# Kernel tuning notes

Measured on AMD Instinct MI355X. Metric: run time of the kernel, lower is better.

The kernel has to match this reference:

```python
import jax, jax.numpy as jnp
import numpy as np
from jax import lax

T, H = 4096, 2048          # tokens, hidden_size
E, K = 64, 8               # n_routed_experts, top_k
I = 512                    # moe_intermediate_size
IS = 512                   # shared intermediate = moe_intermediate_size * n_shared_experts
ROUTED_SCALING = 2.5


def setup_inputs() -> dict:
    key = jax.random.key(0)
    ks = jax.random.split(key, 6)
    return {
        "hidden_states": jax.random.normal(ks[0], (T, H), jnp.float32),
        "gate_w": jax.random.normal(ks[1], (H, E), jnp.float32) * 0.05,
        "w13": jax.random.normal(ks[2], (E, H, 2 * I), jnp.float32) * 0.02,
        "w2": jax.random.normal(ks[3], (E, I, H), jnp.float32) * 0.02,
        "shared_w13": jax.random.normal(ks[4], (H, 2 * IS), jnp.float32) * 0.02,
        "shared_w2": jax.random.normal(ks[5], (IS, H), jnp.float32) * 0.02,
    }


def reference(hidden_states, gate_w, w13, w2, shared_w13, shared_w2):
    # --- router: sigmoid scoring, grouped top-k with 1 group == plain top-k ---
    logits = hidden_states @ gate_w                        # [T, E]
    scores = jax.nn.sigmoid(logits.astype(jnp.float32))
    topk_w, topk_ids = lax.top_k(scores, K)                # [T, K]
    topk_w = topk_w / jnp.sum(topk_w, axis=-1, keepdims=True)  # renormalize

    # --- dispatch: sort token-expert pairs by expert id, grouped GEMM ---
    flat_ids = topk_ids.reshape(-1)                        # [T*K]
    order = jnp.argsort(flat_ids)                          # pairs grouped by expert
    token_idx = order // K                                 # source token of each sorted pair
    x_sorted = hidden_states[token_idx]                    # [T*K, H]
    group_sizes = jnp.bincount(flat_ids, length=E).astype(jnp.int32)

    gu = lax.ragged_dot(x_sorted, w13, group_sizes)        # [T*K, 2I]
    h = jax.nn.silu(gu[:, :I]) * gu[:, I:]                 # SiluAndMul
    out_sorted = lax.ragged_dot(h, w2, group_sizes)        # [T*K, H]

    # --- combine: unsort, weight, sum over top-k ---
    inv = jnp.argsort(order)
    out_pairs = out_sorted[inv].reshape(T, K, H)
    routed = jnp.sum(out_pairs * topk_w[..., None].astype(out_pairs.dtype), axis=1)

    # --- shared expert MLP ---
    sg = hidden_states @ shared_w13                        # [T, 2*IS]
    shared = (jax.nn.silu(sg[:, :IS]) * sg[:, IS:]) @ shared_w2

    return routed * ROUTED_SCALING + shared
```

## Files before the change

kernel.cpp:

```cpp
#include <hip/hip_runtime.h>
#include <hip/hip_bf16.h>

#define T_TOK 4096
#define HD    2048
#define NE    64
#define TOPK  8
#define IMID  512
#define N13   1024
#define NPAIR (T_TOK*TOPK)
#define NROWS (NPAIR + T_TOK)
#define MAXT1 352
#define RSCALE 2.5f

typedef __attribute__((ext_vector_type(8)))  __bf16 bf16x8;
typedef __attribute__((ext_vector_type(4)))  __bf16 bf16x4;
typedef __attribute__((ext_vector_type(4)))  float  f32x4;


__global__ void init_small(int* __restrict__ counts, int* __restrict__ curs) {
  int tid = threadIdx.x;
  if (tid < NE + 1) { counts[tid] = 0; curs[tid] = 0; }
}
__global__ __launch_bounds__(256) void zero_out_kernel(float4* __restrict__ out4) {
  out4[blockIdx.x * 256 + threadIdx.x] = float4{0.f, 0.f, 0.f, 0.f};
}

__global__ __launch_bounds__(256) void logits_kernel(const float* __restrict__ hs,
                                                     const float* __restrict__ gw,
                                                     float* __restrict__ logits,
                                                     __bf16* __restrict__ hidden_bf) {
  __shared__ float hsm[64][16];
  __shared__ float gwm[64][64];
  int tid = threadIdx.x;
  int tb = blockIdx.x * 16;
  int tok = tid >> 4, e4 = (tid & 15) * 4;
  float acc[4] = {0.f, 0.f, 0.f, 0.f};
  for (int c = 0; c < 32; ++c) {
    int kb = c * 64;
    {
      int t16 = tid & 15, kq = tid >> 4;
      float4 f = *(const float4*)&hs[(size_t)(tb + t16) * HD + kb + kq * 4];
      hsm[kq * 4 + 0][t16] = f.x; hsm[kq * 4 + 1][t16] = f.y;
      hsm[kq * 4 + 2][t16] = f.z; hsm[kq * 4 + 3][t16] = f.w;
      bf16x4 hv = { (__bf16)f.x, (__bf16)f.y, (__bf16)f.z, (__bf16)f.w };
      *(bf16x4*)&hidden_bf[(size_t)(tb + t16) * HD + kb + kq * 4] = hv;
#pragma unroll
      for (int it = 0; it < 4; ++it) {
        int q = tid + it * 256;
        int gr = q >> 4, gc = (q & 15) * 4;
        *(float4*)&gwm[gr][gc] = *(const float4*)&gw[(size_t)(kb + gr) * NE + gc];
      }
    }
    __syncthreads();
#pragma unroll 8
    for (int k = 0; k < 64; ++k) {
      float h = hsm[k][tok];
      float4 g = *(const float4*)&gwm[k][e4];
      acc[0] += h * g.x; acc[1] += h * g.y; acc[2] += h * g.z; acc[3] += h * g.w;
    }
    __syncthreads();
  }
#pragma unroll
  for (int j = 0; j < 4; ++j) logits[(size_t)(tb + tok) * NE + e4 + j] = acc[j];
}

__global__ __launch_bounds__(256) void top8_kernel(const float* __restrict__ logits,
                                                   int* __restrict__ topk_id,
                                                   float* __restrict__ pair_w,
                                                   int* __restrict__ counts) {
  int lane = threadIdx.x & 63;
  int t = blockIdx.x * 4 + (threadIdx.x >> 6);
  float v = logits[(size_t)t * NE + lane];
  float s = 1.f / (1.f + __expf(-v));
  float cur = s, ssum = 0.f;
  int myid = 0; float myw = 0.f;
  for (int k = 0; k < TOPK; ++k) {
    float bv = cur; int bi = lane;
#pragma unroll
    for (int off = 32; off >= 1; off >>= 1) {
      float ov = __shfl_xor(bv, off);
      int   oi = __shfl_xor(bi, off);
      if (ov > bv || (ov == bv && oi < bi)) { bv = ov; bi = oi; }
    }
    ssum += bv;
    if (lane == k) { myid = bi; myw = bv; }
    if (lane == bi) cur = -1.f;
  }
  if (lane < TOPK) {
    topk_id[(size_t)t * TOPK + lane] = myid;
    pair_w[(size_t)t * TOPK + lane] = myw / ssum * RSCALE;
    atomicAdd(&counts[myid], 1);
  }
}

__global__ void scan_kernel(const int* __restrict__ counts, int* __restrict__ offs,
                            int2* __restrict__ tiles) {
  __shared__ int cnt[65], pref[66], tp[66];
  int tid = threadIdx.x;
  if (tid < 64) cnt[tid] = counts[tid];
  if (tid == 64) cnt[64] = T_TOK;
  __syncthreads();
  if (tid == 0) {
    int o = 0, t = 0;
    for (int e = 0; e <= 64; ++e) {
      pref[e] = o; tp[e] = t;
      o += cnt[e]; t += (cnt[e] + 127) >> 7;
    }
    pref[65] = o; tp[65] = t;
  }
  __syncthreads();
  if (tid <= 64) {
    offs[tid] = pref[tid];
    int c = cnt[tid], base = pref[tid], tb = tp[tid];
    int nt = (c + 127) >> 7;
    for (int i = 0; i < nt; ++i) {
      int rr = c - i * 128; if (rr > 128) rr = 128;
      tiles[tb + i] = make_int2(base + i * 128, (tid << 16) | rr);
    }
  }
  __syncthreads();
  for (int i = tp[65] + tid; i < MAXT1; i += 128) tiles[i] = make_int2(0, 0);
}

__global__ __launch_bounds__(256) void scatter_kernel(const int* __restrict__ topk_id,
                                                      const float* __restrict__ pair_w,
                                                      const int* __restrict__ offs,
                                                      int* __restrict__ curs,
                                                      int* __restrict__ row_token,
                                                      float* __restrict__ row_w,
                                                      int* __restrict__ inv8) {
  int p = blockIdx.x * 256 + threadIdx.x;
  int dst, t; float w;
  if (p < NPAIR) {
    t = p >> 3; int e = topk_id[p]; w = pair_w[p];
    dst = offs[e] + atomicAdd(&curs[e], 1);
    inv8[p] = dst;
  } else {
    t = p - NPAIR; w = 1.0f;
    dst = NPAIR + t;
  }
  row_token[dst] = t;
  row_w[dst] = w;
}

__device__ __forceinline__ int swz(int row, int kbyte) {
  return row * 128 + (kbyte ^ ((row & 7) << 4));
}
__device__ __forceinline__ void glds16(const void* g, void* l) {
  __builtin_amdgcn_global_load_lds((const __attribute__((address_space(1))) void*)g,
                                   (__attribute__((address_space(3))) void*)l, 16, 0, 0);
}
__device__ __forceinline__ void store_bx8(__bf16* Bs, int col, int kbyte, const float* p) {
  bf16x8 v = { (__bf16)p[0], (__bf16)p[1], (__bf16)p[2], (__bf16)p[3],
               (__bf16)p[4], (__bf16)p[5], (__bf16)p[6], (__bf16)p[7] };
  *(bf16x8*)&Bs[swz(col, kbyte) >> 1] = v;
}

#define G1STEP(S, Acur, Anx2, BGc, BUc, BGn, BUn, RL, RS)                                  \
  {                                                                                        \
    if ((S) + 2 < 32) {                                                                    \
      const float* Bn_ = Bp0 + (size_t)((S) + 2) * 64 * N13;                               \
      _Pragma("unroll") for (int r = 0; r < 16; ++r) RL[r] = Bn_[(size_t)r * N13];         \
      __builtin_amdgcn_sched_barrier(0);                                                   \
      _Pragma("unroll") for (int i = 0; i < 2; ++i)                                        \
        glds16(Abase[i] + ((S) + 2) * 64, (Anx2) + wv * 1024 + i * 512);                   \
    }                                                                                      \
    __builtin_amdgcn_sched_barrier(0);                                                     \
    __builtin_amdgcn_s_setprio(1);                                                         \
    _Pragma("unroll") for (int kk = 0; kk < 2; ++kk) {                                     \
      int koff = kk * 64 + lq * 16;                                                        \
      bf16x8 a[2], bg[2], bu[2];                                                           \
      _Pragma("unroll") for (int i = 0; i < 2; ++i)                                        \
        a[i] = *(const bf16x8*)&(Acur)[swz(wrow * 32 + i * 16 + l15, koff) >> 1];          \
      _Pragma("unroll") for (int j = 0; j < 2; ++j) {                                      \
        bg[j] = *(const bf16x8*)&(BGc)[swz(wc * 32 + j * 16 + l15, koff) >> 1];            \
        bu[j] = *(const bf16x8*)&(BUc)[swz(wc * 32 + j * 16 + l15, koff) >> 1];            \
      }                                                                                    \
      _Pragma("unroll") for (int i = 0; i < 2; ++i)                                        \
        _Pragma("unroll") for (int j = 0; j < 2; ++j) {                                    \
          accg[i][j] = __builtin_amdgcn_mfma_f32_16x16x32_bf16(a[i], bg[j], accg[i][j], 0, 0, 0); \
          accu[i][j] = __builtin_amdgcn_mfma_f32_16x16x32_bf16(a[i], bu[j], accu[i][j], 0, 0, 0); \
        }                                                                                  \
    }                                                                                      \
    __builtin_amdgcn_s_setprio(0);                                                         \
    if ((S) + 1 < 32) {                                                                    \
      __bf16* Bmy_ = bm ? (BUn) : (BGn);                                                   \
      store_bx8(Bmy_, bcol, bkq * 32, RS);                                                 \
      store_bx8(Bmy_, bcol, bkq * 32 + 16, RS + 8);                                        \
    }                                                                                      \
    if ((S) + 2 < 32) asm volatile("s_waitcnt vmcnt(18) lgkmcnt(0)" ::: "memory");         \
    else              asm volatile("s_waitcnt vmcnt(0) lgkmcnt(0)"  ::: "memory");         \
    __builtin_amdgcn_s_barrier();                                                          \
    __builtin_amdgcn_sched_barrier(0);                                                     \
  }

__global__ __launch_bounds__(512, 2) void gemm1_kernel(const __bf16* __restrict__ hidden_bf,
                                                       const float* __restrict__ w13,
                                                       const float* __restrict__ sw13,
                                                       const int* __restrict__ row_token,
                                                       const int2* __restrict__ tiles,
                                                       __bf16* __restrict__ hbuf) {
  int2 td = tiles[blockIdx.y];
  int rows = td.y & 0xFFFF;
  if (rows == 0) return;
  int e = td.y >> 16, row0 = td.x;
  const float* W = (e < NE) ? (w13 + (size_t)e * (HD * N13)) : sw13;
  int n0 = blockIdx.x * 64;

  __shared__ __bf16 As0[128 * 64], As1[128 * 64], As2[128 * 64];
  __shared__ __bf16 Bgs[2][64 * 64];
  __shared__ __bf16 Bus[2][64 * 64];

  int tid = threadIdx.x;
  int lane = tid & 63, wv = tid >> 6;
  int wrow = wv >> 1, wc = wv & 1;
  int l15 = lane & 15, lq = lane >> 4;

  int kswz = (((lane & 7) ^ ((lane >> 3) & 7)) << 3);
  const __bf16* Abase[2];
#pragma unroll
  for (int i = 0; i < 2; ++i) {
    int grow = row0 + wv * 16 + i * 8 + (lane >> 3);
    if (grow >= NROWS) grow = NROWS - 1;
    Abase[i] = hidden_bf + (size_t)row_token[grow] * HD + kswz;
  }
  int bm = tid >> 8, bcol = tid & 63, bkq = (tid >> 6) & 3;
  const float* Bp0 = W + (size_t)(bkq * 16) * N13 + (bm ? 512 + n0 : n0) + bcol;

  float pA[16], pB[16];
#pragma unroll
  for (int r = 0; r < 16; ++r) pA[r] = Bp0[(size_t)r * N13];
  __builtin_amdgcn_sched_barrier(0);
#pragma unroll
  for (int i = 0; i < 2; ++i) glds16(Abase[i], As0 + wv * 1024 + i * 512);
  __builtin_amdgcn_sched_barrier(0);
  {
    const float* B1 = Bp0 + (size_t)64 * N13;
#pragma unroll
    for (int r = 0; r < 16; ++r) pB[r] = B1[(size_t)r * N13];
  }
  __builtin_amdgcn_sched_barrier(0);
#pragma unroll
  for (int i = 0; i < 2; ++i) glds16(Abase[i] + 64, As1 + wv * 1024 + i * 512);
  __builtin_amdgcn_sched_barrier(0);
  {
    __bf16* Bmy = bm ? Bus[0] : Bgs[0];
    store_bx8(Bmy, bcol, bkq * 32, pA);
    store_bx8(Bmy, bcol, bkq * 32 + 16, pA + 8);
  }
  asm volatile("s_waitcnt vmcnt(18) lgkmcnt(0)" ::: "memory");
  __builtin_amdgcn_s_barrier();
  __builtin_amdgcn_sched_barrier(0);

  f32x4 accg[2][2], accu[2][2];
#pragma unroll
  for (int i = 0; i < 2; ++i)
#pragma unroll
    for (int j = 0; j < 2; ++j) { accg[i][j] = (f32x4)(0.f); accu[i][j] = (f32x4)(0.f); }

  __bf16 *Ac = As0, *A1 = As1, *A2 = As2;
  for (int s = 0; s < 32; s += 2) {
    G1STEP(s,     Ac, A2, Bgs[0], Bus[0], Bgs[1], Bus[1], pA, pB);
    { __bf16* t = Ac; Ac = A1; A1 = A2; A2 = t; }
    G1STEP(s + 1, Ac, A2, Bgs[1], Bus[1], Bgs[0], Bus[0], pB, pA);
    { __bf16* t = Ac; Ac = A1; A1 = A2; A2 = t; }
  }
#pragma unroll
  for (int mi = 0; mi < 2; ++mi) {
#pragma unroll
    for (int r = 0; r < 4; ++r) {
      int rl = wrow * 32 + mi * 16 + lq * 4 + r;
      if (rl < rows) {
        size_t hrow = (size_t)(row0 + rl) * IMID;
#pragma unroll
        for (int j = 0; j < 2; ++j) {
          float g = accg[mi][j][r], u = accu[mi][j][r];
          float hv = g * u / (1.f + __expf(-g));
          hbuf[hrow + n0 + wc * 32 + j * 16 + l15] = (__bf16)hv;
        }
      }
    }
  }
}

#define G2STEP(S, Acur, Anx2, Bc, Bn, RL, RS)                                              \
  {                                                                                        \
    if ((S) + 2 < 8) {                                                                     \
      const float* Bn_ = Bp0 + (size_t)((S) + 2) * 64 * HD;                                \
      _Pragma("unroll") for (int r = 0; r < 16; ++r) RL[r] = Bn_[(size_t)r * HD];          \
      __builtin_amdgcn_sched_barrier(0);                                                   \
      _Pragma("unroll") for (int i = 0; i < 2; ++i)                                        \
        glds16(Abase[i] + ((S) + 2) * 64, (Anx2) + wv * 1024 + i * 512);                   \
    }                                                                                      \
    __builtin_amdgcn_sched_barrier(0);                                                     \
    __builtin_amdgcn_s_setprio(1);                                                         \
    _Pragma("unroll") for (int kk = 0; kk < 2; ++kk) {                                     \
      int koff = kk * 64 + lq * 16;                                                        \
      bf16x8 a[2], b[4];                                                                   \
      _Pragma("unroll") for (int i = 0; i < 2; ++i)                                        \
        a[i] = *(const bf16x8*)&(Acur)[swz(wrow * 32 + i * 16 + l15, koff) >> 1];          \
      _Pragma("unroll") for (int j = 0; j < 4; ++j)                                        \
        b[j] = *(const bf16x8*)&(Bc)[swz(wc * 64 + j * 16 + l15, koff) >> 1];              \
      _Pragma("unroll") for (int i = 0; i < 2; ++i)                                        \
        _Pragma("unroll") for (int j = 0; j < 4; ++j)                                      \
          acc[i][j] = __builtin_amdgcn_mfma_f32_16x16x32_bf16(a[i], b[j], acc[i][j], 0, 0, 0); \
    }                                                                                      \
    __builtin_amdgcn_s_setprio(0);                                                         \
    if ((S) + 1 < 8) {                                                                     \
      store_bx8((Bn), bcol, bkq * 32, RS);                                                 \
      store_bx8((Bn), bcol, bkq * 32 + 16, RS + 8);                                        \
    }                                                                                      \
    if ((S) + 2 < 8) asm volatile("s_waitcnt vmcnt(18) lgkmcnt(0)" ::: "memory");          \
    else             asm volatile("s_waitcnt vmcnt(0) lgkmcnt(0)"  ::: "memory");          \
    __builtin_amdgcn_s_barrier();                                                          \
    __builtin_amdgcn_sched_barrier(0);                                                     \
  }

template<int MODE>
__global__ __launch_bounds__(512, 2) void gemm2_kernel(const __bf16* __restrict__ hbuf,
                                                       const float* __restrict__ w2,
                                                       const float* __restrict__ sw2,
                                                       const int* __restrict__ row_token,
                                                       const float* __restrict__ row_w,
                                                       const int2* __restrict__ tiles,
                                                       void* __restrict__ dstv) {
  int2 td = tiles[blockIdx.y];
  int rows = td.y & 0xFFFF;
  if (rows == 0) return;
  int e = td.y >> 16, row0 = td.x;
  const float* W = (e < NE) ? (w2 + (size_t)e * (IMID * HD)) : sw2;
  int n0 = blockIdx.x * 128;

  __shared__ __bf16 As0[128 * 64], As1[128 * 64], As2[128 * 64];
  __shared__ __bf16 Bs[2][128 * 64];

  int tid = threadIdx.x;
  int lane = tid & 63, wv = tid >> 6;
  int wrow = wv >> 1, wc = wv & 1;
  int l15 = lane & 15, lq = lane >> 4;

  int kswz = (((lane & 7) ^ ((lane >> 3) & 7)) << 3);
  const __bf16* Abase[2];
#pragma unroll
  for (int i = 0; i < 2; ++i) {
    int grow = row0 + wv * 16 + i * 8 + (lane >> 3);
    if (grow >= NROWS) grow = NROWS - 1;
    Abase[i] = hbuf + (size_t)grow * IMID + kswz;
  }
  int bcol = tid & 127, bkq = tid >> 7;
  const float* Bp0 = W + (size_t)(bkq * 16) * HD + n0 + bcol;

  float pA[16], pB[16];
#pragma unroll
  for (int r = 0; r < 16; ++r) pA[r] = Bp0[(size_t)r * HD];
  __builtin_amdgcn_sched_barrier(0);
#pragma unroll
  for (int i = 0; i < 2; ++i) glds16(Abase[i], As0 + wv * 1024 + i * 512);
  __builtin_amdgcn_sched_barrier(0);
  {
    const float* B1 = Bp0 + (size_t)64 * HD;
#pragma unroll
    for (int r = 0; r < 16; ++r) pB[r] = B1[(size_t)r * HD];
  }
  __builtin_amdgcn_sched_barrier(0);
#pragma unroll
  for (int i = 0; i < 2; ++i) glds16(Abase[i] + 64, As1 + wv * 1024 + i * 512);
  __builtin_amdgcn_sched_barrier(0);
  store_bx8(Bs[0], bcol, bkq * 32, pA);
  store_bx8(Bs[0], bcol, bkq * 32 + 16, pA + 8);
  asm volatile("s_waitcnt vmcnt(18) lgkmcnt(0)" ::: "memory");
  __builtin_amdgcn_s_barrier();
  __builtin_amdgcn_sched_barrier(0);

  f32x4 acc[2][4];
#pragma unroll
  for (int i = 0; i < 2; ++i)
#pragma unroll
    for (int j = 0; j < 4; ++j) acc[i][j] = (f32x4)(0.f);

  __bf16 *Ac = As0, *A1 = As1, *A2 = As2;
  for (int s = 0; s < 8; s += 2) {
    G2STEP(s,     Ac, A2, Bs[0], Bs[1], pA, pB);
    { __bf16* t = Ac; Ac = A1; A1 = A2; A2 = t; }
    G2STEP(s + 1, Ac, A2, Bs[1], Bs[0], pB, pA);
    { __bf16* t = Ac; Ac = A1; A1 = A2; A2 = t; }
  }
#pragma unroll
  for (int mi = 0; mi < 2; ++mi) {
#pragma unroll
    for (int r = 0; r < 4; ++r) {
      int rl = wrow * 32 + mi * 16 + lq * 4 + r;
      if (rl < rows) {
        int gr = row0 + rl;
        float wgt = row_w[gr];
        if (MODE == 1) {
          __bf16* prow = (__bf16*)dstv + (size_t)gr * HD + n0 + wc * 64;
#pragma unroll
          for (int j = 0; j < 4; ++j)
            prow[j * 16 + l15] = (__bf16)(acc[mi][j][r] * wgt);
        } else {
          int tok = row_token[gr];
          float* orow = (float*)dstv + (size_t)tok * HD + n0 + wc * 64;
#pragma unroll
          for (int j = 0; j < 4; ++j)
            atomicAdd(&orow[j * 16 + l15], acc[mi][j][r] * wgt);
        }
      }
    }
  }
}

__global__ __launch_bounds__(256) void combine_kernel(const __bf16* __restrict__ pairout,
                                                      const int* __restrict__ inv8,
                                                      float* __restrict__ out) {
  int t = blockIdx.x;
  int c = threadIdx.x * 8;
  float s0 = 0.f, s1 = 0.f, s2 = 0.f, s3 = 0.f, s4 = 0.f, s5 = 0.f, s6 = 0.f, s7 = 0.f;
#pragma unroll
  for (int k = 0; k < 8; ++k) {
    bf16x8 v = *(const bf16x8*)(pairout + (size_t)inv8[t * 8 + k] * HD + c);
    s0 += (float)v[0]; s1 += (float)v[1]; s2 += (float)v[2]; s3 += (float)v[3];
    s4 += (float)v[4]; s5 += (float)v[5]; s6 += (float)v[6]; s7 += (float)v[7];
  }
  {
    bf16x8 v = *(const bf16x8*)(pairout + (size_t)(NPAIR + t) * HD + c);
    s0 += (float)v[0]; s1 += (float)v[1]; s2 += (float)v[2]; s3 += (float)v[3];
    s4 += (float)v[4]; s5 += (float)v[5]; s6 += (float)v[6]; s7 += (float)v[7];
  }
  float4* o = (float4*)(out + (size_t)t * HD + c);
  o[0] = float4{s0, s1, s2, s3};
  o[1] = float4{s4, s5, s6, s7};
}

extern "C" void kernel_launch(void* const* d_in, const int* in_sizes, int n_in,
                              void* d_out, int out_size, void* d_ws, size_t ws_size,
                              hipStream_t stream) {
  const float* hidden = (const float*)d_in[0];
  const float* gate_w = (const float*)d_in[1];
  const float* w13    = (const float*)d_in[2];
  const float* w2     = (const float*)d_in[3];
  const float* sw13   = (const float*)d_in[4];
  const float* sw2    = (const float*)d_in[5];
  float* out = (float*)d_out;

  char* ws = (char*)d_ws;
  size_t off = 0;
  __bf16* hbuf      = (__bf16*)(ws + off); off += (size_t)NROWS * IMID * 2;
  __bf16* hidden_bf = (__bf16*)(ws + off); off += (size_t)T_TOK * HD * 2;
  float* logits  = (float*)(ws + off);  off += (size_t)T_TOK * NE * 4;
  int*   topk_id = (int*)(ws + off);    off += (size_t)NPAIR * 4;
  float* pair_w  = (float*)(ws + off);  off += (size_t)NPAIR * 4;
  int*   row_tok = (int*)(ws + off);    off += (size_t)NROWS * 4;
  float* row_w   = (float*)(ws + off);  off += (size_t)NROWS * 4;
  int*   inv8    = (int*)(ws + off);    off += (size_t)NPAIR * 4;
  int*   counts  = (int*)(ws + off);    off += 512;
  int*   curs    = (int*)(ws + off);    off += 512;
  int*   offs    = (int*)(ws + off);    off += 512;
  int2*  tiles   = (int2*)(ws + off);   off += MAXT1 * 8;
  off = (off + 255) & ~(size_t)255;
  __bf16* pairout = (__bf16*)(ws + off);
  size_t need_rows = off + (size_t)NROWS * HD * 2;
  bool rows_path = (ws_size >= need_rows);

  init_small<<<1, 256, 0, stream>>>(counts, curs);
  if (!rows_path)
    zero_out_kernel<<<T_TOK * HD / 4 / 256, 256, 0, stream>>>((float4*)out);
  logits_kernel<<<T_TOK / 16, 256, 0, stream>>>(hidden, gate_w, logits, hidden_bf);
  top8_kernel<<<T_TOK / 4, 256, 0, stream>>>(logits, topk_id, pair_w, counts);
  scan_kernel<<<1, 128, 0, stream>>>(counts, offs, tiles);
  scatter_kernel<<<NROWS / 256, 256, 0, stream>>>(topk_id, pair_w, offs, curs,
                                                  row_tok, row_w, inv8);
  gemm1_kernel<<<dim3(8, MAXT1), 512, 0, stream>>>(hidden_bf, w13, sw13, row_tok, tiles, hbuf);
  if (rows_path) {
    gemm2_kernel<1><<<dim3(16, MAXT1), 512, 0, stream>>>(hbuf, w2, sw2, row_tok, row_w,
                                                         tiles, (void*)pairout);
    combine_kernel<<<T_TOK, 256, 0, stream>>>(pairout, inv8, out);
  } else {
    gemm2_kernel<0><<<dim3(16, MAXT1), 512, 0, stream>>>(hbuf, w2, sw2, row_tok, row_w,
                                                         tiles, (void*)out);
  }
}
```

Baseline: 709.3 us.

## Convert w2 to bf16 inside gemm1 extra blocks so gemm2 streams half-width weights

Adds extra blocks to the gemm1 launch that convert the fp32 routed and shared w2 weights into a bf16 copy in workspace. gemm2 is templated on the weight type and reads this bf16 copy, halving the bytes each tile pulls for B. The conversion is redone on every call, costing a full read of w2 (about 268MB) plus a bf16 write inside gemm1. It only runs when the workspace is large enough.

```diff
diff --git a/kernel.cpp b/kernel.cpp
--- a/kernel.cpp
+++ b/kernel.cpp
@@ -10,7 +10,10 @@
 #define NPAIR (T_TOK*TOPK)
 #define NROWS (NPAIR + T_TOK)
 #define MAXT1 352
+#define CVTY  32
 #define RSCALE 2.5f
+#define W2ELEMS  ((size_t)NE * IMID * HD)
+#define SW2ELEMS ((size_t)IMID * HD)
 
 typedef __attribute__((ext_vector_type(8)))  __bf16 bf16x8;
 typedef __attribute__((ext_vector_type(4)))  __bf16 bf16x4;
@@ -153,6 +156,10 @@
 __device__ __forceinline__ void store_bx8(__bf16* Bs, int col, int kbyte, const float* p) {
   bf16x8 v = { (__bf16)p[0], (__bf16)p[1], (__bf16)p[2], (__bf16)p[3],
                (__bf16)p[4], (__bf16)p[5], (__bf16)p[6], (__bf16)p[7] };
+  *(bf16x8*)&Bs[swz(col, kbyte) >> 1] = v;
+}
+__device__ __forceinline__ void store_bx8(__bf16* Bs, int col, int kbyte, const __bf16* p) {
+  bf16x8 v = { p[0], p[1], p[2], p[3], p[4], p[5], p[6], p[7] };
   *(bf16x8*)&Bs[swz(col, kbyte) >> 1] = v;
 }
 
@@ -194,12 +201,29 @@
     __builtin_amdgcn_sched_barrier(0);                                                     \
   }
 
+template<int DOCVT>
 __global__ __launch_bounds__(512, 2) void gemm1_kernel(const __bf16* __restrict__ hidden_bf,
                                                        const float* __restrict__ w13,
                                                        const float* __restrict__ sw13,
                                                        const int* __restrict__ row_token,
                                                        const int2* __restrict__ tiles,
-                                                       __bf16* __restrict__ hbuf) {
+                                                       __bf16* __restrict__ hbuf,
+                                                       const float* __restrict__ w2f,
+                                                       const float* __restrict__ sw2f,
+                                                       __bf16* __restrict__ wdst) {
+  if (DOCVT && blockIdx.y >= MAXT1) {
+    int cb = (blockIdx.y - MAXT1) * 8 + blockIdx.x;
+    const size_t NV = (W2ELEMS + SW2ELEMS) / 8;
+    for (size_t v = (size_t)cb * 512 + threadIdx.x; v < NV; v += (size_t)256 * 512) {
+      size_t base = v * 8;
+      const float* src = (base < W2ELEMS) ? (w2f + base) : (sw2f + (base - W2ELEMS));
+      float4 a = *(const float4*)src, b = *(const float4*)(src + 4);
+      bf16x8 o = { (__bf16)a.x, (__bf16)a.y, (__bf16)a.z, (__bf16)a.w,
+                   (__bf16)b.x, (__bf16)b.y, (__bf16)b.z, (__bf16)b.w };
+      *(bf16x8*)(wdst + base) = o;
+    }
+    return;
+  }
   int2 td = tiles[blockIdx.y];
   int rows = td.y & 0xFFFF;
   if (rows == 0) return;
@@ -286,7 +310,7 @@
 #define G2STEP(S, Acur, Anx2, Bc, Bn, RL, RS)                                              \
   {                                                                                        \
     if ((S) + 2 < 8) {                                                                     \
-      const float* Bn_ = Bp0 + (size_t)((S) + 2) * 64 * HD;                                \
+      const TB* Bn_ = Bp0 + (size_t)((S) + 2) * 64 * HD;                                   \
       _Pragma("unroll") for (int r = 0; r < 16; ++r) RL[r] = Bn_[(size_t)r * HD];          \
       __builtin_amdgcn_sched_barrier(0);                                                   \
       _Pragma("unroll") for (int i = 0; i < 2; ++i)                                        \
@@ -316,10 +340,10 @@
     __builtin_amdgcn_sched_barrier(0);                                                     \
   }
 
-template<int MODE>
+template<typename TB, int MODE>
 __global__ __launch_bounds__(512, 2) void gemm2_kernel(const __bf16* __restrict__ hbuf,
-                                                       const float* __restrict__ w2,
-                                                       const float* __restrict__ sw2,
+                                                       const TB* __restrict__ w2,
+                                                       const TB* __restrict__ sw2,
                                                        const int* __restrict__ row_token,
                                                        const float* __restrict__ row_w,
                                                        const int2* __restrict__ tiles,
@@ -328,7 +352,7 @@
   int rows = td.y & 0xFFFF;
   if (rows == 0) return;
   int e = td.y >> 16, row0 = td.x;
-  const float* W = (e < NE) ? (w2 + (size_t)e * (IMID * HD)) : sw2;
+  const TB* W = (e < NE) ? (w2 + (size_t)e * (IMID * HD)) : sw2;
   int n0 = blockIdx.x * 128;
 
   __shared__ __bf16 As0[128 * 64], As1[128 * 64], As2[128 * 64];
@@ -348,9 +372,9 @@
     Abase[i] = hbuf + (size_t)grow * IMID + kswz;
   }
   int bcol = tid & 127, bkq = tid >> 7;
-  const float* Bp0 = W + (size_t)(bkq * 16) * HD + n0 + bcol;
-
-  float pA[16], pB[16];
+  const TB* Bp0 = W + (size_t)(bkq * 16) * HD + n0 + bcol;
+
+  TB pA[16], pB[16];
 #pragma unroll
   for (int r = 0; r < 16; ++r) pA[r] = Bp0[(size_t)r * HD];
   __builtin_amdgcn_sched_barrier(0);
@@ -358,7 +382,7 @@
   for (int i = 0; i < 2; ++i) glds16(Abase[i], As0 + wv * 1024 + i * 512);
   __builtin_amdgcn_sched_barrier(0);
   {
-    const float* B1 = Bp0 + (size_t)64 * HD;
+    const TB* B1 = Bp0 + (size_t)64 * HD;
 #pragma unroll
     for (int r = 0; r < 16; ++r) pB[r] = B1[(size_t)r * HD];
   }
@@ -461,6 +485,9 @@
   __bf16* pairout = (__bf16*)(ws + off);
   size_t need_rows = off + (size_t)NROWS * HD * 2;
   bool rows_path = (ws_size >= need_rows);
+  size_t woff = (need_rows + 255) & ~(size_t)255;
+  __bf16* w2b = (__bf16*)(ws + woff);
+  bool wfit = rows_path && (ws_size >= woff + (W2ELEMS + SW2ELEMS) * 2);
 
   init_small<<<1, 256, 0, stream>>>(counts, curs);
   if (!rows_path)
@@ -470,13 +497,22 @@
   scan_kernel<<<1, 128, 0, stream>>>(counts, offs, tiles);
   scatter_kernel<<<NROWS / 256, 256, 0, stream>>>(topk_id, pair_w, offs, curs,
                                                   row_tok, row_w, inv8);
-  gemm1_kernel<<<dim3(8, MAXT1), 512, 0, stream>>>(hidden_bf, w13, sw13, row_tok, tiles, hbuf);
-  if (rows_path) {
-    gemm2_kernel<1><<<dim3(16, MAXT1), 512, 0, stream>>>(hbuf, w2, sw2, row_tok, row_w,
-                                                         tiles, (void*)pairout);
+  if (wfit) {
+    gemm1_kernel<1><<<dim3(8, MAXT1 + CVTY), 512, 0, stream>>>(
+        hidden_bf, w13, sw13, row_tok, tiles, hbuf, w2, sw2, w2b);
+    gemm2_kernel<__bf16, 1><<<dim3(16, MAXT1), 512, 0, stream>>>(
+        hbuf, w2b, w2b + W2ELEMS, row_tok, row_w, tiles, (void*)pairout);
     combine_kernel<<<T_TOK, 256, 0, stream>>>(pairout, inv8, out);
   } else {
-    gemm2_kernel<0><<<dim3(16, MAXT1), 512, 0, stream>>>(hbuf, w2, sw2, row_tok, row_w,
-                                                         tiles, (void*)out);
-  }
-}
+    gemm1_kernel<0><<<dim3(8, MAXT1), 512, 0, stream>>>(
+        hidden_bf, w13, sw13, row_tok, tiles, hbuf, nullptr, nullptr, nullptr);
+    if (rows_path) {
+      gemm2_kernel<float, 1><<<dim3(16, MAXT1), 512, 0, stream>>>(
+          hbuf, w2, sw2, row_tok, row_w, tiles, (void*)pairout);
+      combine_kernel<<<T_TOK, 256, 0, stream>>>(pairout, inv8, out);
+    } else {
+      gemm2_kernel<float, 0><<<dim3(16, MAXT1), 512, 0, stream>>>(
+          hbuf, w2, sw2, row_tok, row_w, tiles, (void*)out);
+    }
+  }
+}
```

After: 752.8 us. 1.06x slower.
